# Performance work log

Hardware: AMD Instinct MI355X
Metric: run time of the kernel (lower is better)

The kernel has to match this reference:

```python
import jax, jax.numpy as jnp
import numpy as np

B, S, HID = 2, 2048, 2048
NH, NOPE, ROPE = 16, 128, 64
HD = NOPE + ROPE          # 192
VHD = 128
KVR, QR = 512, 1536
FFN = 5632
THETA = 10000.0
EPS = 1e-6


def rmsnorm(x, w, eps=EPS):
    xf = x.astype(jnp.float32)
    rms = jnp.sqrt(jnp.mean(xf * xf, axis=-1, keepdims=True) + eps)
    return (xf / rms).astype(x.dtype) * w


def apply_rope(x, cos, sin):
    # x: (..., rope_dim); half-split rotation convention
    half = x.shape[-1] // 2
    x1, x2 = x[..., :half], x[..., half:]
    return jnp.concatenate([x1 * cos - x2 * sin, x2 * cos + x1 * sin], axis=-1)


def rope_tables(seq_len, dim, theta=THETA):
    inv_freq = 1.0 / (theta ** (jnp.arange(0, dim, 2, dtype=jnp.float32) / dim))
    t = jnp.arange(seq_len, dtype=jnp.float32)
    freqs = jnp.outer(t, inv_freq)           # (S, dim/2)
    return jnp.cos(freqs), jnp.sin(freqs)


def setup_inputs():
    key = jax.random.key(0)
    ks = jax.random.split(key, 10)
    def w(k, shape, fan_in):
        return jax.random.normal(k, shape, dtype=jnp.float32) * (fan_in ** -0.5)
    return {
        'x': jax.random.normal(ks[0], (B, S, HID), dtype=jnp.float32),
        'attn_norm_w': jnp.ones((HID,), jnp.float32),
        'wq_down': w(ks[1], (HID, QR), HID),
        'wq_up': w(ks[2], (QR, NH * HD), QR),
        'wkv_down': w(ks[3], (HID, KVR + ROPE), HID),
        'kv_norm_w': jnp.ones((KVR,), jnp.float32),
        'wkv_up': w(ks[4], (KVR, NH * (NOPE + VHD)), KVR),
        'wout': w(ks[5], (NH * VHD, HID), NH * VHD),
        'ffn_norm_w': jnp.ones((HID,), jnp.float32),
        'w_gate': w(ks[6], (HID, FFN), HID),
        'w_up': w(ks[7], (HID, FFN), HID),
        'w_down': w(ks[8], (FFN, HID), FFN),
    }


def reference(x, attn_norm_w, wq_down, wq_up, wkv_down, kv_norm_w, wkv_up, wout,
              ffn_norm_w, w_gate, w_up, w_down):
    scale = 1.0 / np.sqrt(HD)
    # --- attention sub-block ---
    h = rmsnorm(x, attn_norm_w)
    q = (h @ wq_down) @ wq_up                       # (B,S,NH*HD)
    q = q.reshape(B, S, NH, HD)
    q_nope, q_rope = q[..., :NOPE], q[..., NOPE:]
    kv_full = h @ wkv_down                          # (B,S,KVR+ROPE)
    kv_c, k_rope = kv_full[..., :KVR], kv_full[..., KVR:]
    kv_c = rmsnorm(kv_c, kv_norm_w)
    kv_exp = (kv_c @ wkv_up).reshape(B, S, NH, NOPE + VHD)
    k_nope, v = kv_exp[..., :NOPE], kv_exp[..., NOPE:]

    cos, sin = rope_tables(S, ROPE)                 # (S, ROPE/2)
    cos4, sin4 = cos[None, :, None, :], sin[None, :, None, :]
    q_rope = apply_rope(q_rope, cos4, sin4)         # (B,S,NH,ROPE)
    k_rope = apply_rope(k_rope[:, :, None, :], cos4, sin4)  # (B,S,1,ROPE)
    k_rope = jnp.broadcast_to(k_rope, (B, S, NH, ROPE))

    q_full = jnp.concatenate([q_nope, q_rope], axis=-1)     # (B,S,NH,HD)
    k = jnp.concatenate([k_nope, k_rope], axis=-1)          # (B,S,NH,HD)

    scores = jnp.einsum('bqhd,bkhd->bhqk', q_full, k) * scale
    causal = jnp.tril(jnp.ones((S, S), dtype=bool))
    scores = jnp.where(causal[None, None], scores, jnp.finfo(scores.dtype).min)
    probs = jax.nn.softmax(scores, axis=-1)
    attn = jnp.einsum('bhqk,bkhd->bqhd', probs, v).reshape(B, S, NH * VHD)
    x = x + attn @ wout

    # --- SwiGLU MLP sub-block ---
    h2 = rmsnorm(x, ffn_norm_w)
    ffn = (jax.nn.silu(h2 @ w_gate) * (h2 @ w_up)) @ w_down
    return x + ffn
```

## Files before the change

kernel.cpp:

```cpp
#include <hip/hip_runtime.h>
#include <hip/hip_bf16.h>


using bf16x8 = __attribute__((ext_vector_type(8))) short;
using f32x4  = __attribute__((ext_vector_type(4))) float;

#define GLOBAL_AS __attribute__((address_space(1)))
#define LDS_AS    __attribute__((address_space(3)))
#define MFMA16(a, b, c) __builtin_amdgcn_mfma_f32_16x16x32_bf16((a), (b), (c), 0, 0, 0)

static constexpr int Sc = 2048;

__device__ __forceinline__ void gload16(const void* g, void* l) {
  __builtin_amdgcn_global_load_lds((const GLOBAL_AS unsigned int*)g,
                                   (LDS_AS unsigned int*)l, 16, 0, 0);
}
__device__ __forceinline__ float bf2f(unsigned short u) {
  union { float f; unsigned int i; } x; x.i = ((unsigned int)u) << 16; return x.f;
}
__device__ __forceinline__ unsigned short f2bf(float f) {
  union { float f; unsigned int i; } x; x.f = f;
  unsigned int i = x.i;
  return (unsigned short)((i + 0x7fffu + ((i >> 16) & 1u)) >> 16);
}
__device__ __forceinline__ int swz4(int r) { return ((r >> 2) & 3) ^ (r & 3); }

__global__ void fill_k(float* out, float v, int n) {
  int i = blockIdx.x * 256 + threadIdx.x;
  if (i < n) out[i] = v;
}

__global__ __launch_bounds__(256) void wtrans(const float* __restrict__ W,
                                              unsigned short* __restrict__ WT,
                                              int K, int N) {
  __shared__ float t[64][65];
  const int n0 = blockIdx.x * 64, k0 = blockIdx.y * 64;
  const int tx = threadIdx.x & 15, ty = threadIdx.x >> 4;
#pragma unroll
  for (int i = 0; i < 4; ++i) {
    int k = k0 + ty + i * 16;
    const float4 v = *(const float4*)(W + (size_t)k * N + n0 + tx * 4);
    t[ty + i * 16][tx * 4 + 0] = v.x;
    t[ty + i * 16][tx * 4 + 1] = v.y;
    t[ty + i * 16][tx * 4 + 2] = v.z;
    t[ty + i * 16][tx * 4 + 3] = v.w;
  }
  __syncthreads();
  const int kx = threadIdx.x & 7, ny = threadIdx.x >> 3;
#pragma unroll
  for (int i = 0; i < 2; ++i) {
    int nl = ny + i * 32;
    unsigned short u[8];
#pragma unroll
    for (int j = 0; j < 8; ++j) u[j] = f2bf(t[kx * 8 + j][nl]);
    *(uint4*)(WT + (size_t)(n0 + nl) * K + k0 + kx * 8) = *(uint4*)u;
  }
}

__global__ void rope_tab(float* __restrict__ cosT, float* __restrict__ sinT) {
  int i = blockIdx.x * 256 + threadIdx.x;
  if (i >= Sc * 32) return;
  int s = i >> 5, j = i & 31;
  float inv = powf(10000.0f, -(float)j / 32.0f);
  float a = (float)s * inv;
  cosT[i] = cosf(a);
  sinT[i] = sinf(a);
}

__global__ __launch_bounds__(256) void rmsnorm_k(const float* __restrict__ in,
                                                 const float* __restrict__ w,
                                                 unsigned short* __restrict__ out,
                                                 int D, int istride, int ostride) {
  const int row = blockIdx.x;
  const float* x = in + (size_t)row * istride;
  float ss = 0.f;
  for (int c = threadIdx.x * 4; c < D; c += 1024) {
    const float4 v = *(const float4*)(x + c);
    ss += v.x * v.x + v.y * v.y + v.z * v.z + v.w * v.w;
  }
#pragma unroll
  for (int off = 1; off < 64; off <<= 1) ss += __shfl_xor(ss, off);
  __shared__ float part[4];
  if ((threadIdx.x & 63) == 0) part[threadIdx.x >> 6] = ss;
  __syncthreads();
  float tot = part[0] + part[1] + part[2] + part[3];
  float r = rsqrtf(tot / (float)D + 1e-6f);
  for (int c = threadIdx.x * 4; c < D; c += 1024) {
    const float4 v = *(const float4*)(x + c);
    ushort4 o;
    o.x = f2bf(v.x * r * w[c + 0]);
    o.y = f2bf(v.y * r * w[c + 1]);
    o.z = f2bf(v.z * r * w[c + 2]);
    o.w = f2bf(v.w * r * w[c + 3]);
    *(ushort4*)(out + (size_t)row * ostride + c) = o;
  }
}

enum { EPI_BF16 = 0, EPI_F32 = 1, EPI_ADDF32 = 2, EPI_SILU = 3 };

template <int EPI>
__global__ __launch_bounds__(256) void gemm_sb1(const unsigned short* __restrict__ A,
                                                const unsigned short* __restrict__ BT,
                                                void* __restrict__ Cp,
                                                const float* __restrict__ resid,
                                                const unsigned short* __restrict__ other,
                                                int M, int N, int K) {
  __shared__ unsigned short ldsA[128 * 64];
  __shared__ unsigned short ldsB[128 * 64];
  const int tid = threadIdx.x;
  const int w = tid >> 6, lane = tid & 63;
  const int rl = lane & 15, gh = lane >> 4;
  const int wm = (w >> 1) * 64, wn = (w & 1) * 64;

  const int nwg = gridDim.x;
  const int orig = blockIdx.x;
  const int qq = nwg >> 3, rr = nwg & 7;
  const int xcd = orig & 7, lidx = orig >> 3;
  const int fswz = (xcd < rr ? xcd * (qq + 1) : rr * (qq + 1) + (xcd - rr) * qq) + lidx;
  const int MT = M >> 7;
  const int m0 = (fswz % MT) * 128;
  const int n0 = (fswz / MT) * 128;

  const unsigned short* sA[4];
  const unsigned short* sB[4];
#pragma unroll
  for (int i = 0; i < 4; ++i) {
    int G = i * 256 + tid, r = G >> 3, sl = (G & 7) ^ (r & 7);
    sA[i] = A + (size_t)(m0 + r) * K + sl * 8;
    sB[i] = BT + (size_t)(n0 + r) * K + sl * 8;
  }
  auto STAGE = [&](int kt) {
    const int ko = kt * 64;
#pragma unroll
    for (int i = 0; i < 4; ++i) {
      gload16(sA[i] + ko, &ldsA[(i * 256 + w * 64) * 8]);
      gload16(sB[i] + ko, &ldsB[(i * 256 + w * 64) * 8]);
    }
  };

  int aoff[4], boff[4];
#pragma unroll
  for (int i = 0; i < 4; ++i) {
    aoff[i] = (wm + i * 16 + rl) * 64;
    boff[i] = (wn + i * 16 + rl) * 64;
  }

  f32x4 acc[4][4] = {};
  const int nk = K >> 6;

  STAGE(0);
  asm volatile("s_waitcnt vmcnt(0)" ::: "memory");
  __builtin_amdgcn_s_barrier();

  for (int kt = 0; kt < nk; ++kt) {
    bf16x8 a[4][2], b[4][2];
#pragma unroll
    for (int i = 0; i < 4; ++i)
#pragma unroll
      for (int ks = 0; ks < 2; ++ks) {
        const int ra = wm + i * 16 + rl;
        a[i][ks] = *(const bf16x8*)&ldsA[aoff[i] + ((((ks << 2) + gh)) ^ (ra & 7)) * 8];
        const int rb = wn + i * 16 + rl;
        b[i][ks] = *(const bf16x8*)&ldsB[boff[i] + ((((ks << 2) + gh)) ^ (rb & 7)) * 8];
      }
    __builtin_amdgcn_s_setprio(1);
#pragma unroll
    for (int ks = 0; ks < 2; ++ks)
#pragma unroll
      for (int i = 0; i < 4; ++i)
#pragma unroll
        for (int j = 0; j < 4; ++j) acc[i][j] = MFMA16(a[i][ks], b[j][ks], acc[i][j]);
    __builtin_amdgcn_s_setprio(0);
    asm volatile("s_waitcnt lgkmcnt(0)" ::: "memory");
    __builtin_amdgcn_sched_barrier(0);
    __builtin_amdgcn_s_barrier();
    STAGE((kt + 1 < nk) ? kt + 1 : nk - 1);
    asm volatile("s_waitcnt vmcnt(0)" ::: "memory");
    __builtin_amdgcn_sched_barrier(0);
    __builtin_amdgcn_s_barrier();
  }

#pragma unroll
  for (int i = 0; i < 4; ++i) {
#pragma unroll
    for (int j = 0; j < 4; ++j) {
#pragma unroll
      for (int rg = 0; rg < 4; ++rg) {
        const int row = m0 + wm + i * 16 + gh * 4 + rg;
        const int col = n0 + wn + j * 16 + rl;
        const size_t idx = (size_t)row * N + col;
        const float v = acc[i][j][rg];
        if constexpr (EPI == EPI_BF16) {
          ((unsigned short*)Cp)[idx] = f2bf(v);
        } else if constexpr (EPI == EPI_F32) {
          ((float*)Cp)[idx] = v;
        } else if constexpr (EPI == EPI_ADDF32) {
          ((float*)Cp)[idx] = v + resid[idx];
        } else {
          float gv = bf2f(other[idx]);
          float sg = gv / (1.f + __expf(-gv));
          ((unsigned short*)Cp)[idx] = f2bf(sg * v);
        }
      }
    }
  }
}

template <int EPI>
__global__ __launch_bounds__(256) void gemm_bt(const unsigned short* __restrict__ A,
                                               const unsigned short* __restrict__ BT,
                                               void* __restrict__ Cp,
                                               const float* __restrict__ resid,
                                               const unsigned short* __restrict__ other,
                                               int M, int N, int K) {
  __shared__ unsigned short ldsA[2][128 * 32];
  __shared__ unsigned short ldsB[2][128 * 32];
  const int tid = threadIdx.x;
  const int w = tid >> 6, lane = tid & 63;
  const int nwg = gridDim.x;
  const int orig = blockIdx.x;
  const int qq = nwg >> 3, rr = nwg & 7;
  const int xcd = orig & 7, lidx = orig >> 3;
  const int fswz = (xcd < rr ? xcd * (qq + 1) : rr * (qq + 1) + (xcd - rr) * qq) + lidx;
  const int m0 = (fswz & 31) * 128;
  const int n0 = (fswz >> 5) * 128;

  const int wm = (w >> 1) * 64, wn = (w & 1) * 64;
  const int rl = lane & 15, gsel = lane >> 4;

  const int p0 = w * 64 + lane;
  const int p1 = p0 + 256;
  const int r0 = p0 >> 2, r1 = p1 >> 2;
  const int g0 = (p0 & 3) ^ swz4(r0), g1 = (p1 & 3) ^ swz4(r1);
  const unsigned short* gA0 = A + (size_t)(m0 + r0) * K + g0 * 8;
  const unsigned short* gA1 = A + (size_t)(m0 + r1) * K + g1 * 8;
  const unsigned short* gB0 = BT + (size_t)(n0 + r0) * K + g0 * 8;
  const unsigned short* gB1 = BT + (size_t)(n0 + r1) * K + g1 * 8;
  const int dA0 = (w * 64) * 8, dA1 = dA0 + 2048;

  int aoff[4], boff[4];
#pragma unroll
  for (int i = 0; i < 4; ++i) {
    int ra = wm + i * 16 + rl;
    aoff[i] = ra * 32 + (gsel ^ swz4(ra)) * 8;
    int rb = wn + i * 16 + rl;
    boff[i] = rb * 32 + (gsel ^ swz4(rb)) * 8;
  }

  auto STAGE = [&](int kt, int p) {
    const int ko = kt * 32;
    gload16(gA0 + ko, &ldsA[p][dA0]);
    gload16(gA1 + ko, &ldsA[p][dA1]);
    gload16(gB0 + ko, &ldsB[p][dA0]);
    gload16(gB1 + ko, &ldsB[p][dA1]);
  };

  f32x4 acc[4][4] = {};
  const int nk = K >> 5;

  STAGE(0, 0);
  STAGE(1, 1);
  for (int kt = 0; kt < nk; ++kt) {
    asm volatile("s_waitcnt vmcnt(4)" ::: "memory");
    __builtin_amdgcn_s_barrier();
    __builtin_amdgcn_sched_barrier(0);
    const unsigned short* lA = &ldsA[kt & 1][0];
    const unsigned short* lB = &ldsB[kt & 1][0];
    bf16x8 a[4], b[4];
#pragma unroll
    for (int i = 0; i < 4; ++i) a[i] = *(const bf16x8*)&lA[aoff[i]];
#pragma unroll
    for (int i = 0; i < 4; ++i) b[i] = *(const bf16x8*)&lB[boff[i]];
    __builtin_amdgcn_s_setprio(1);
#pragma unroll
    for (int i = 0; i < 4; ++i)
#pragma unroll
      for (int j = 0; j < 4; ++j) acc[i][j] = MFMA16(a[i], b[j], acc[i][j]);
    __builtin_amdgcn_s_setprio(0);
    __builtin_amdgcn_sched_barrier(0);
    __builtin_amdgcn_s_barrier();
    const int nxt = (kt + 2 < nk) ? kt + 2 : nk - 1;
    STAGE(nxt, kt & 1);
  }

#pragma unroll
  for (int i = 0; i < 4; ++i) {
#pragma unroll
    for (int j = 0; j < 4; ++j) {
#pragma unroll
      for (int rg = 0; rg < 4; ++rg) {
        const int row = m0 + wm + i * 16 + gsel * 4 + rg;
        const int col = n0 + wn + j * 16 + rl;
        const size_t idx = (size_t)row * N + col;
        const float v = acc[i][j][rg];
        if constexpr (EPI == EPI_BF16) {
          ((unsigned short*)Cp)[idx] = f2bf(v);
        } else if constexpr (EPI == EPI_F32) {
          ((float*)Cp)[idx] = v;
        } else if constexpr (EPI == EPI_ADDF32) {
          ((float*)Cp)[idx] = v + resid[idx];
        } else {
          float gv = bf2f(other[idx]);
          float sg = gv / (1.f + __expf(-gv));
          ((unsigned short*)Cp)[idx] = f2bf(sg * v);
        }
      }
    }
  }
}

__global__ __launch_bounds__(256) void repack_q(const unsigned short* __restrict__ q,
                                                const float* __restrict__ cosT,
                                                const float* __restrict__ sinT,
                                                unsigned short* __restrict__ Qc) {
  const int row = blockIdx.x;
  const int b = row >> 11, s = row & 2047;
  const float scale = 0.07216878364870322f;
  const unsigned short* qr = q + (size_t)row * 3072;
  for (int i = threadIdx.x; i < 3072; i += 256) {
    int h = i / 192, d = i - h * 192;
    float v;
    if (d < 128) {
      v = bf2f(qr[h * 192 + d]);
    } else {
      int j = d - 128;
      int jj = j & 31;
      float x1 = bf2f(qr[h * 192 + 128 + jj]);
      float x2 = bf2f(qr[h * 192 + 160 + jj]);
      float c = cosT[s * 32 + jj], sn = sinT[s * 32 + jj];
      v = (j < 32) ? (x1 * c - x2 * sn) : (x2 * c + x1 * sn);
    }
    Qc[((size_t)(b * 16 + h) * Sc + s) * 192 + d] = f2bf(v * scale);
  }
}

__global__ __launch_bounds__(256) void repack_kv(const unsigned short* __restrict__ kvex,
                                                 const float* __restrict__ kvf,
                                                 const float* __restrict__ cosT,
                                                 const float* __restrict__ sinT,
                                                 unsigned short* __restrict__ Kc,
                                                 unsigned short* __restrict__ VT) {
  __shared__ unsigned short vt_lds[32][136];
  const int bid = blockIdx.x;
  const int st = bid & 63;
  const int h = (bid >> 6) & 15;
  const int b = bid >> 10;
  const int s0 = st * 32;
  const int tid = threadIdx.x;
  const size_t KcBase = (size_t)(b * 16 + h) * Sc;
  for (int i = tid; i < 32 * 32; i += 256) {
    int r = i >> 5, g = i & 31;
    uint4 vdat = *(const uint4*)(kvex + (size_t)(b * Sc + s0 + r) * 4096 + h * 256 + g * 8);
    if (g < 16) {
      *(uint4*)(Kc + (KcBase + s0 + r) * 192 + g * 8) = vdat;
    } else {
      *(uint4*)(&vt_lds[r][(g - 16) * 8]) = vdat;
    }
  }
  for (int i = tid; i < 32 * 64; i += 256) {
    int r = i >> 6, d = i & 63;
    int s = s0 + r;
    int jj = d & 31;
    const float* kvrow = kvf + (size_t)(b * Sc + s) * 640;
    float x1 = kvrow[512 + jj], x2 = kvrow[544 + jj];
    float c = cosT[s * 32 + jj], sn = sinT[s * 32 + jj];
    float v = (d < 32) ? (x1 * c - x2 * sn) : (x2 * c + x1 * sn);
    Kc[(KcBase + s) * 192 + 128 + d] = f2bf(v);
  }
  __syncthreads();
  const int f = tid >> 1, sh = (tid & 1) * 16;
  unsigned int vals[8];
#pragma unroll
  for (int k2 = 0; k2 < 8; ++k2) {
    unsigned int lo = vt_lds[sh + 2 * k2][f];
    unsigned int hi = vt_lds[sh + 2 * k2 + 1][f];
    vals[k2] = lo | (hi << 16);
  }
  unsigned short* dst = VT + ((size_t)(b * 16 + h) * 128 + f) * Sc + s0 + sh;
  ((uint4*)dst)[0] = make_uint4(vals[0], vals[1], vals[2], vals[3]);
  ((uint4*)dst)[1] = make_uint4(vals[4], vals[5], vals[6], vals[7]);
}

__global__ __launch_bounds__(512) void attn_k(const unsigned short* __restrict__ Qc,
                                              const unsigned short* __restrict__ Kc,
                                              const unsigned short* __restrict__ VT,
                                              unsigned short* __restrict__ Ob) {
  __shared__ unsigned short lds_k[2][64 * 192];
  __shared__ unsigned short lds_v[2][128 * 64];
  __shared__ __align__(16) unsigned short p_lds[8][16 * 72];
  const int tid = threadIdx.x, w = tid >> 6, lane = tid & 63;
  const int rl = lane & 15, gh = lane >> 4;
  const int bidx = blockIdx.x;
  const int bh = bidx & 31;
  const int qt = 15 - (bidx >> 5);
  const unsigned short* Qh = Qc + (size_t)bh * Sc * 192;
  const unsigned short* Kh = Kc + (size_t)bh * Sc * 192;
  const unsigned short* Vh = VT + (size_t)bh * 128 * Sc;
  const int qr0 = qt * 128 + w * 16;

  bf16x8 qf[6];
#pragma unroll
  for (int kk = 0; kk < 6; ++kk)
    qf[kk] = *(const bf16x8*)(Qh + (size_t)(qr0 + rl) * 192 + kk * 32 + gh * 8);

  f32x4 o[8] = {};
  float mrun[4] = {-1e30f, -1e30f, -1e30f, -1e30f};
  float srun[4] = {0.f, 0.f, 0.f, 0.f};

  int kr[3], kg[3];
#pragma unroll
  for (int j = 0; j < 3; ++j) {
    int G = j * 512 + tid;
    int r = G / 24, gq = G - r * 24;
    kr[j] = r;
    kg[j] = (gq & ~7) | ((gq & 7) ^ (r & 7));
  }
  int vr[2], vg[2];
#pragma unroll
  for (int j = 0; j < 2; ++j) {
    int G = j * 512 + tid;
    int r = G >> 3;
    vr[j] = r;
    vg[j] = (G & 7) ^ (r & 7);
  }

  auto STAGE = [&](int t, int b) {
    const int k0 = t * 64;
#pragma unroll
    for (int j = 0; j < 3; ++j)
      gload16(Kh + (size_t)(k0 + kr[j]) * 192 + kg[j] * 8,
              &lds_k[b][(j * 512 + w * 64) * 8]);
#pragma unroll
    for (int j = 0; j < 2; ++j)
      gload16(Vh + (size_t)vr[j] * Sc + k0 + vg[j] * 8,
              &lds_v[b][(j * 512 + w * 64) * 8]);
  };

  STAGE(0, 0);
  asm volatile("s_waitcnt vmcnt(0)" ::: "memory");
  __builtin_amdgcn_s_barrier();
  __builtin_amdgcn_sched_barrier(0);

  const int nt = 2 * qt + 2;
  int cur = 0;
  for (int t = 0; t < nt; ++t) {
    if (t + 1 < nt) STAGE(t + 1, cur ^ 1);
    const int k0 = t * 64;
    if (k0 <= qr0 + 15) {
      const unsigned short* lk = lds_k[cur];
      const unsigned short* lv = lds_v[cur];
      f32x4 s[4] = {};
      __builtin_amdgcn_s_setprio(1);
#pragma unroll
      for (int kk = 0; kk < 6; ++kk) {
        const int gq = kk * 4 + gh;
#pragma unroll
        for (int ks = 0; ks < 4; ++ks) {
          const int krow = ks * 16 + rl;
          const int ph = (gq & ~7) | ((gq & 7) ^ (krow & 7));
          bf16x8 kf = *(const bf16x8*)&lk[krow * 192 + ph * 8];
          s[ks] = MFMA16(qf[kk], kf, s[ks]);
        }
      }
      __builtin_amdgcn_s_setprio(0);
      if (k0 + 63 > qr0) {
#pragma unroll
        for (int ks = 0; ks < 4; ++ks)
#pragma unroll
          for (int rg = 0; rg < 4; ++rg) {
            int qrow = qr0 + gh * 4 + rg;
            if (k0 + ks * 16 + rl > qrow) s[ks][rg] = -1e30f;
          }
      }
      float tmax[4];
#pragma unroll
      for (int rg = 0; rg < 4; ++rg) {
        float v = fmaxf(fmaxf(s[0][rg], s[1][rg]), fmaxf(s[2][rg], s[3][rg]));
        v = fmaxf(v, __shfl_xor(v, 1));
        v = fmaxf(v, __shfl_xor(v, 2));
        v = fmaxf(v, __shfl_xor(v, 4));
        v = fmaxf(v, __shfl_xor(v, 8));
        tmax[rg] = v;
      }
      int need = !(tmax[0] <= mrun[0] + 8.f && tmax[1] <= mrun[1] + 8.f &&
                   tmax[2] <= mrun[2] + 8.f && tmax[3] <= mrun[3] + 8.f);
      if (__any(need)) {
        float al[4];
#pragma unroll
        for (int rg = 0; rg < 4; ++rg) {
          float mn = fmaxf(mrun[rg], tmax[rg]);
          al[rg] = __expf(mrun[rg] - mn);
          mrun[rg] = mn;
          srun[rg] *= al[rg];
        }
#pragma unroll
        for (int i = 0; i < 8; ++i)
#pragma unroll
          for (int rg = 0; rg < 4; ++rg) o[i][rg] *= al[rg];
      }
      unsigned short* pw = p_lds[w];
#pragma unroll
      for (int ks = 0; ks < 4; ++ks)
#pragma unroll
        for (int rg = 0; rg < 4; ++rg) {
          float p = __expf(s[ks][rg] - mrun[rg]);
          srun[rg] += p;
          pw[(gh * 4 + rg) * 72 + ks * 16 + rl] = f2bf(p);
        }
      bf16x8 pa0 = *(const bf16x8*)&pw[rl * 72 + 0 * 32 + gh * 8];
      bf16x8 pa1 = *(const bf16x8*)&pw[rl * 72 + 1 * 32 + gh * 8];
      __builtin_amdgcn_s_setprio(1);
#pragma unroll
      for (int vf = 0; vf < 8; ++vf) {
        const int row = vf * 16 + rl;
        bf16x8 v0 = *(const bf16x8*)&lv[row * 64 + ((0 * 4 + gh) ^ (row & 7)) * 8];
        o[vf] = MFMA16(pa0, v0, o[vf]);
        bf16x8 v1 = *(const bf16x8*)&lv[row * 64 + ((1 * 4 + gh) ^ (row & 7)) * 8];
        o[vf] = MFMA16(pa1, v1, o[vf]);
      }
      __builtin_amdgcn_s_setprio(0);
    }
    asm volatile("s_waitcnt vmcnt(0)" ::: "memory");
    __builtin_amdgcn_s_barrier();
    __builtin_amdgcn_sched_barrier(0);
    cur ^= 1;
  }
  float rd[4];
#pragma unroll
  for (int rg = 0; rg < 4; ++rg) {
    float rs = srun[rg];
    rs += __shfl_xor(rs, 1);
    rs += __shfl_xor(rs, 2);
    rs += __shfl_xor(rs, 4);
    rs += __shfl_xor(rs, 8);
    rd[rg] = 1.f / rs;
  }
  const int b = bh >> 4, hh = bh & 15;
#pragma unroll
  for (int vf = 0; vf < 8; ++vf) {
#pragma unroll
    for (int rg = 0; rg < 4; ++rg) {
      int srow = qr0 + gh * 4 + rg;
      int col = hh * 128 + vf * 16 + rl;
      Ob[((size_t)(b * Sc) + srow) * 2048 + col] = f2bf(o[vf][rg] * rd[rg]);
    }
  }
}

extern "C" void kernel_launch(void* const* d_in, const int* in_sizes, int n_in,
                              void* d_out, int out_size, void* d_ws, size_t ws_size,
                              hipStream_t stream) {
  (void)in_sizes; (void)n_in;
  const float* x    = (const float*)d_in[0];
  const float* anw  = (const float*)d_in[1];
  const float* wqd  = (const float*)d_in[2];
  const float* wqu  = (const float*)d_in[3];
  const float* wkvd = (const float*)d_in[4];
  const float* kvnw = (const float*)d_in[5];
  const float* wkvu = (const float*)d_in[6];
  const float* wout = (const float*)d_in[7];
  const float* fnw  = (const float*)d_in[8];
  const float* wg   = (const float*)d_in[9];
  const float* wu   = (const float*)d_in[10];
  const float* wd   = (const float*)d_in[11];
  float* out = (float*)d_out;

  char* ws = (char*)d_ws;
  size_t off = 0;
  auto alloc = [&](size_t bytes) -> char* {
    char* p = ws + off;
    off += (bytes + 255) & ~(size_t)255;
    return p;
  };
  unsigned short* wslot = (unsigned short*)alloc(5632ull * 2048 * 2);
  float* cosT           = (float*)alloc(2048ull * 32 * 4);
  float* sinT           = (float*)alloc(2048ull * 32 * 4);
  unsigned short* hbuf  = (unsigned short*)alloc(4096ull * 2048 * 2);
  char* arena           = alloc(4096ull * 1536 * 2 + 4096ull * 3072 * 2);
  float* kvf            = (float*)alloc(4096ull * 640 * 4);
  unsigned short* kvn   = (unsigned short*)alloc(4096ull * 512 * 2);
  unsigned short* Qc    = (unsigned short*)alloc(32ull * 2048 * 192 * 2);
  unsigned short* Kc    = (unsigned short*)alloc(32ull * 2048 * 192 * 2);
  unsigned short* VTb   = (unsigned short*)alloc(32ull * 128 * 2048 * 2);
  const size_t NEED = off;

  if (ws_size < NEED) {
    fill_k<<<dim3((out_size + 255) / 256), dim3(256), 0, stream>>>(
        out, (float)(ws_size >> 20), out_size);
    return;
  }

  unsigned short* qd    = (unsigned short*)arena;
  unsigned short* q     = (unsigned short*)(arena + 4096ull * 1536 * 2);
  unsigned short* kvex  = (unsigned short*)arena;
  unsigned short* h     = hbuf;
  unsigned short* attnb = hbuf;
  unsigned short* h2    = hbuf;
  unsigned short* gbuf  = Qc;
  float* x2             = out;

  dim3 blk(256), blk512(512);
  rope_tab<<<dim3(256), blk, 0, stream>>>(cosT, sinT);
  rmsnorm_k<<<dim3(4096), blk, 0, stream>>>(x, anw, h, 2048, 2048, 2048);

  wtrans<<<dim3(24, 32), blk, 0, stream>>>(wqd, wslot, 2048, 1536);
  gemm_sb1<EPI_BF16><<<dim3(32 * 12), blk, 0, stream>>>(h, wslot, qd, nullptr, nullptr, 4096, 1536, 2048);
  wtrans<<<dim3(48, 24), blk, 0, stream>>>(wqu, wslot, 1536, 3072);
  gemm_sb1<EPI_BF16><<<dim3(32 * 24), blk, 0, stream>>>(qd, wslot, q, nullptr, nullptr, 4096, 3072, 1536);
  repack_q<<<dim3(4096), blk, 0, stream>>>(q, cosT, sinT, Qc);

  wtrans<<<dim3(9, 32), blk, 0, stream>>>(wkvd, wslot, 2048, 576);
  gemm_bt<EPI_F32><<<dim3(5 * 32), blk, 0, stream>>>(h, wslot, kvf, nullptr, nullptr, 4096, 640, 2048);
  rmsnorm_k<<<dim3(4096), blk, 0, stream>>>(kvf, kvnw, kvn, 512, 640, 512);
  wtrans<<<dim3(64, 8), blk, 0, stream>>>(wkvu, wslot, 512, 4096);
  gemm_sb1<EPI_BF16><<<dim3(32 * 32), blk, 0, stream>>>(kvn, wslot, kvex, nullptr, nullptr, 4096, 4096, 512);
  repack_kv<<<dim3(2048), blk, 0, stream>>>(kvex, kvf, cosT, sinT, Kc, VTb);

  attn_k<<<dim3(512), blk512, 0, stream>>>(Qc, Kc, VTb, attnb);
  wtrans<<<dim3(32, 32), blk, 0, stream>>>(wout, wslot, 2048, 2048);
  gemm_sb1<EPI_ADDF32><<<dim3(32 * 16), blk, 0, stream>>>(attnb, wslot, x2, x, nullptr, 4096, 2048, 2048);

  rmsnorm_k<<<dim3(4096), blk, 0, stream>>>(x2, fnw, h2, 2048, 2048, 2048);
  wtrans<<<dim3(88, 32), blk, 0, stream>>>(wg, wslot, 2048, 5632);
  gemm_sb1<EPI_BF16><<<dim3(32 * 44), blk, 0, stream>>>(h2, wslot, gbuf, nullptr, nullptr, 4096, 5632, 2048);
  wtrans<<<dim3(88, 32), blk, 0, stream>>>(wu, wslot, 2048, 5632);
  gemm_sb1<EPI_SILU><<<dim3(32 * 44), blk, 0, stream>>>(h2, wslot, gbuf, nullptr, gbuf, 4096, 5632, 2048);
  wtrans<<<dim3(32, 88), blk, 0, stream>>>(wd, wslot, 5632, 2048);
  gemm_sb1<EPI_ADDF32><<<dim3(32 * 16), blk, 0, stream>>>(gbuf, wslot, out, x2, nullptr, 4096, 2048, 5632);
}
```

Baseline: 785.0 us.

## Double-buffer LDS tiles in main GEMM to overlap loads with MFMA

The single-buffered GEMM kernel becomes a double-buffered one. The next K tile's global-to-LDS loads are issued into the alternate buffer before the current tile's MFMAs run, and one barrier per iteration is removed. This hides global load latency behind compute. In exchange, LDS use doubles to 64KB per block, which may lower occupancy.

```diff
diff --git a/kernel.cpp b/kernel.cpp
--- a/kernel.cpp
+++ b/kernel.cpp
@@ -99,14 +99,14 @@
 enum { EPI_BF16 = 0, EPI_F32 = 1, EPI_ADDF32 = 2, EPI_SILU = 3 };
 
 template <int EPI>
-__global__ __launch_bounds__(256) void gemm_sb1(const unsigned short* __restrict__ A,
-                                                const unsigned short* __restrict__ BT,
-                                                void* __restrict__ Cp,
-                                                const float* __restrict__ resid,
-                                                const unsigned short* __restrict__ other,
-                                                int M, int N, int K) {
-  __shared__ unsigned short ldsA[128 * 64];
-  __shared__ unsigned short ldsB[128 * 64];
+__global__ __launch_bounds__(256) void gemm_db(const unsigned short* __restrict__ A,
+                                               const unsigned short* __restrict__ BT,
+                                               void* __restrict__ Cp,
+                                               const float* __restrict__ resid,
+                                               const unsigned short* __restrict__ other,
+                                               int M, int N, int K) {
+  __shared__ unsigned short ldsA[2][128 * 64];
+  __shared__ unsigned short ldsB[2][128 * 64];
   const int tid = threadIdx.x;
   const int w = tid >> 6, lane = tid & 63;
   const int rl = lane & 15, gh = lane >> 4;
@@ -129,12 +129,12 @@
     sA[i] = A + (size_t)(m0 + r) * K + sl * 8;
     sB[i] = BT + (size_t)(n0 + r) * K + sl * 8;
   }
-  auto STAGE = [&](int kt) {
+  auto STAGE = [&](int kt, int p) {
     const int ko = kt * 64;
 #pragma unroll
     for (int i = 0; i < 4; ++i) {
-      gload16(sA[i] + ko, &ldsA[(i * 256 + w * 64) * 8]);
-      gload16(sB[i] + ko, &ldsB[(i * 256 + w * 64) * 8]);
+      gload16(sA[i] + ko, &ldsA[p][(i * 256 + w * 64) * 8]);
+      gload16(sB[i] + ko, &ldsB[p][(i * 256 + w * 64) * 8]);
     }
   };
 
@@ -148,20 +148,24 @@
   f32x4 acc[4][4] = {};
   const int nk = K >> 6;
 
-  STAGE(0);
+  STAGE(0, 0);
   asm volatile("s_waitcnt vmcnt(0)" ::: "memory");
   __builtin_amdgcn_s_barrier();
 
   for (int kt = 0; kt < nk; ++kt) {
+    const int cur = kt & 1, nx = cur ^ 1;
+    STAGE((kt + 1 < nk) ? kt + 1 : nk - 1, nx);
+    const unsigned short* lA = &ldsA[cur][0];
+    const unsigned short* lB = &ldsB[cur][0];
     bf16x8 a[4][2], b[4][2];
 #pragma unroll
     for (int i = 0; i < 4; ++i)
 #pragma unroll
       for (int ks = 0; ks < 2; ++ks) {
         const int ra = wm + i * 16 + rl;
-        a[i][ks] = *(const bf16x8*)&ldsA[aoff[i] + ((((ks << 2) + gh)) ^ (ra & 7)) * 8];
+        a[i][ks] = *(const bf16x8*)&lA[aoff[i] + ((((ks << 2) + gh)) ^ (ra & 7)) * 8];
         const int rb = wn + i * 16 + rl;
-        b[i][ks] = *(const bf16x8*)&ldsB[boff[i] + ((((ks << 2) + gh)) ^ (rb & 7)) * 8];
+        b[i][ks] = *(const bf16x8*)&lB[boff[i] + ((((ks << 2) + gh)) ^ (rb & 7)) * 8];
       }
     __builtin_amdgcn_s_setprio(1);
 #pragma unroll
@@ -172,9 +176,6 @@
         for (int j = 0; j < 4; ++j) acc[i][j] = MFMA16(a[i][ks], b[j][ks], acc[i][j]);
     __builtin_amdgcn_s_setprio(0);
     asm volatile("s_waitcnt lgkmcnt(0)" ::: "memory");
-    __builtin_amdgcn_sched_barrier(0);
-    __builtin_amdgcn_s_barrier();
-    STAGE((kt + 1 < nk) ? kt + 1 : nk - 1);
     asm volatile("s_waitcnt vmcnt(0)" ::: "memory");
     __builtin_amdgcn_sched_barrier(0);
     __builtin_amdgcn_s_barrier();
@@ -604,27 +605,27 @@
   rmsnorm_k<<<dim3(4096), blk, 0, stream>>>(x, anw, h, 2048, 2048, 2048);
 
   wtrans<<<dim3(24, 32), blk, 0, stream>>>(wqd, wslot, 2048, 1536);
-  gemm_sb1<EPI_BF16><<<dim3(32 * 12), blk, 0, stream>>>(h, wslot, qd, nullptr, nullptr, 4096, 1536, 2048);
+  gemm_db<EPI_BF16><<<dim3(32 * 12), blk, 0, stream>>>(h, wslot, qd, nullptr, nullptr, 4096, 1536, 2048);
   wtrans<<<dim3(48, 24), blk, 0, stream>>>(wqu, wslot, 1536, 3072);
-  gemm_sb1<EPI_BF16><<<dim3(32 * 24), blk, 0, stream>>>(qd, wslot, q, nullptr, nullptr, 4096, 3072, 1536);
+  gemm_db<EPI_BF16><<<dim3(32 * 24), blk, 0, stream>>>(qd, wslot, q, nullptr, nullptr, 4096, 3072, 1536);
   repack_q<<<dim3(4096), blk, 0, stream>>>(q, cosT, sinT, Qc);
 
   wtrans<<<dim3(9, 32), blk, 0, stream>>>(wkvd, wslot, 2048, 576);
   gemm_bt<EPI_F32><<<dim3(5 * 32), blk, 0, stream>>>(h, wslot, kvf, nullptr, nullptr, 4096, 640, 2048);
   rmsnorm_k<<<dim3(4096), blk, 0, stream>>>(kvf, kvnw, kvn, 512, 640, 512);
   wtrans<<<dim3(64, 8), blk, 0, stream>>>(wkvu, wslot, 512, 4096);
-  gemm_sb1<EPI_BF16><<<dim3(32 * 32), blk, 0, stream>>>(kvn, wslot, kvex, nullptr, nullptr, 4096, 4096, 512);
+  gemm_db<EPI_BF16><<<dim3(32 * 32), blk, 0, stream>>>(kvn, wslot, kvex, nullptr, nullptr, 4096, 4096, 512);
   repack_kv<<<dim3(2048), blk, 0, stream>>>(kvex, kvf, cosT, sinT, Kc, VTb);
 
   attn_k<<<dim3(512), blk512, 0, stream>>>(Qc, Kc, VTb, attnb);
   wtrans<<<dim3(32, 32), blk, 0, stream>>>(wout, wslot, 2048, 2048);
-  gemm_sb1<EPI_ADDF32><<<dim3(32 * 16), blk, 0, stream>>>(attnb, wslot, x2, x, nullptr, 4096, 2048, 2048);
+  gemm_db<EPI_ADDF32><<<dim3(32 * 16), blk, 0, stream>>>(attnb, wslot, x2, x, nullptr, 4096, 2048, 2048);
 
   rmsnorm_k<<<dim3(4096), blk, 0, stream>>>(x2, fnw, h2, 2048, 2048, 2048);
   wtrans<<<dim3(88, 32), blk, 0, stream>>>(wg, wslot, 2048, 5632);
-  gemm_sb1<EPI_BF16><<<dim3(32 * 44), blk, 0, stream>>>(h2, wslot, gbuf, nullptr, nullptr, 4096, 5632, 2048);
+  gemm_db<EPI_BF16><<<dim3(32 * 44), blk, 0, stream>>>(h2, wslot, gbuf, nullptr, nullptr, 4096, 5632, 2048);
   wtrans<<<dim3(88, 32), blk, 0, stream>>>(wu, wslot, 2048, 5632);
-  gemm_sb1<EPI_SILU><<<dim3(32 * 44), blk, 0, stream>>>(h2, wslot, gbuf, nullptr, gbuf, 4096, 5632, 2048);
+  gemm_db<EPI_SILU><<<dim3(32 * 44), blk, 0, stream>>>(h2, wslot, gbuf, nullptr, gbuf, 4096, 5632, 2048);
   wtrans<<<dim3(32, 88), blk, 0, stream>>>(wd, wslot, 5632, 2048);
-  gemm_sb1<EPI_ADDF32><<<dim3(32 * 16), blk, 0, stream>>>(gbuf, wslot, out, x2, nullptr, 4096, 2048, 5632);
-}
+  gemm_db<EPI_ADDF32><<<dim3(32 * 16), blk, 0, stream>>>(gbuf, wslot, out, x2, nullptr, 4096, 2048, 5632);
+}
```

After: 786.4 us. Within noise of the previous version (+0.2%).
